# Kernel tuning notes

Hardware: AMD Instinct MI355X
Metric: run time of the kernel (lower is better)

Reference implementation:

```python
import jax, jax.numpy as jnp
import numpy as np

D = 256

def setup_inputs() -> dict:
    key = jax.random.key(0)
    ks = iter(jax.random.split(key, 40))
    def nrm(shape, s=0.05):
        return (jax.random.normal(next(ks), shape, dtype=jnp.float32) * s)
    inp = {}
    inp['prot_data'] = jax.random.normal(next(ks), (8, 1000, 768), dtype=jnp.float32)
    inp['drug_data_ver'] = jax.random.normal(next(ks), (8, 56, 43), dtype=jnp.float32)
    inp['drug_data_adj'] = jax.random.uniform(next(ks), (8, 56, 56), dtype=jnp.float32)
    inp['prot_contacts'] = jax.random.uniform(next(ks), (8, 1000, 1000), dtype=jnp.float32)
    inp['prot_inter'] = jax.random.uniform(next(ks), (8, 1000, 56), dtype=jnp.float32)
    inp['prot_inter_exist'] = jax.random.uniform(next(ks), (8,), dtype=jnp.float32)
    inp['label'] = jax.random.normal(next(ks), (8, 1), dtype=jnp.float32)
    inp['fused_matrix'] = jax.random.normal(next(ks), (999, 1000), dtype=jnp.float32)
    # params
    inp['W_prot'] = nrm((768, D)); inp['b_prot'] = jnp.zeros((D,), jnp.float32)
    inp['gcn_W0'] = nrm((43, D));  inp['gcn_b0'] = jnp.zeros((D,), jnp.float32)
    inp['gcn_W1'] = nrm((D, D));   inp['gcn_b1'] = jnp.zeros((D,), jnp.float32)
    inp['gcn_W2'] = nrm((D, D));   inp['gcn_b2'] = jnp.zeros((D,), jnp.float32)
    inp['gcn_Wf'] = nrm((D, D));   inp['gcn_bf'] = jnp.zeros((D,), jnp.float32)
    inp['Wjp'] = nrm((D, D)); inp['bjp'] = jnp.zeros((D,), jnp.float32)
    inp['Wjc'] = nrm((D, D)); inp['bjc'] = jnp.zeros((D,), jnp.float32)
    inp['conv_w'] = nrm((64, 1, 4)); inp['conv_b'] = jnp.zeros((64,), jnp.float32)
    inp['W_r1'] = nrm((64 * 32, 600)); inp['b_r1'] = jnp.zeros((600,), jnp.float32)
    inp['W_r2'] = nrm((600, 300));     inp['b_r2'] = jnp.zeros((300,), jnp.float32)
    inp['W_r3'] = nrm((300, 1));       inp['b_r3'] = jnp.zeros((1,), jnp.float32)
    return inp

LAM_L1 = 1.0; LAM_FUSED = 1.0; LAM_GROUP = 1.0; LAM_BIND = 1.0

def reference(prot_data, drug_data_ver, drug_data_adj, prot_contacts, prot_inter,
              prot_inter_exist, label, fused_matrix,
              W_prot, b_prot, gcn_W0, gcn_b0, gcn_W1, gcn_b1, gcn_W2, gcn_b2,
              gcn_Wf, gcn_bf, Wjp, bjp, Wjc, bjc, conv_w, conv_b,
              W_r1, b_r1, W_r2, b_r2, W_r3, b_r3):
    # protein embedding (active path: single linear)
    prot = prot_data @ W_prot + b_prot                      # (b, 1000, 256)
    # compound GCN
    x = drug_data_ver
    for W, b in ((gcn_W0, gcn_b0), (gcn_W1, gcn_b1), (gcn_W2, gcn_b2)):
        x = jax.nn.relu(jnp.einsum('bij,bjd->bid', drug_data_adj, x @ W + b))
    comp = x @ gcn_Wf + gcn_bf                              # (b, 56, 256)
    # joint attention over prot x comp
    qp = jax.nn.relu(prot) @ Wjp + bjp
    qc = jax.nn.relu(comp) @ Wjc + bjc
    inter = jax.nn.sigmoid(jnp.einsum('bid,bkd->bik', qp, qc))  # (b, 1000, 56)
    inter = inter / jnp.sum(inter, axis=(1, 2), keepdims=True)
    # outer-product bilinear attention + weighted reduction (the 4D intermediate)
    cp4 = jnp.tanh(prot[:, :, None, :] * comp[:, None, :, :])   # (b, 1000, 56, 256)
    cp = jnp.einsum('bikd,bik->bd', cp4, inter)                 # (b, 256)
    h = cp[:, None, :]                                          # (b, 1, 256) NCH
    h = jax.lax.conv_general_dilated(h, conv_w, (2,), [(1, 1)],
                                     dimension_numbers=('NCH', 'OIH', 'NCH'))
    h = h + conv_b[None, :, None]                               # (b, 64, 128)
    h = jax.nn.leaky_relu(h, 0.1)
    h = jax.lax.reduce_window(h, -jnp.inf, jax.lax.max,
                              (1, 1, 4), (1, 1, 4), 'VALID')    # (b, 64, 32)
    h = h.reshape(h.shape[0], 64 * 32)
    h = jax.nn.leaky_relu(h @ W_r1 + b_r1, 0.1)
    h = jax.nn.leaky_relu(h @ W_r2 + b_r2, 0.1)
    affn = h @ W_r3 + b_r3                                      # (b, 1)
    # losses
    reg_l1 = jnp.mean(jnp.sum(jnp.abs(inter), axis=(1, 2)))
    reg_fused = jnp.mean(jnp.sum(jnp.abs(jnp.einsum('bij,ti->bjt', inter, fused_matrix)), axis=(1, 2)))
    group = jnp.sum(jnp.einsum('bij,bki->bjk', inter ** 2, prot_contacts), axis=1)  # (b, 1000)
    group = jnp.where(group == 0, group + 1e10, group)
    reg_group = jnp.mean(jnp.sum(jnp.sqrt(group) * jnp.sqrt(jnp.sum(prot_contacts, axis=2)), axis=1))
    loss0 = LAM_L1 * reg_l1 + LAM_FUSED * reg_fused + LAM_GROUP * reg_group
    lab_inter = prot_inter_exist[:, None, None] * prot_inter
    loss1 = jnp.mean(jnp.sqrt(jnp.sum((inter - lab_inter) ** 2, axis=(1, 2)))) * LAM_BIND
    loss2 = jnp.mean((affn - label) ** 2)
    return loss0 + loss1 + loss2
```

## Files before the change

### kernel.cpp

```cpp
#include <hip/hip_runtime.h>
#include <hip/hip_bf16.h>
#include <math.h>

#define B 8
#define NP 1000
#define NK 56
#define DP 768
#define DV 43
#define DD 256
#define NT 999

typedef __attribute__((ext_vector_type(8))) short bf16x8;
typedef __attribute__((ext_vector_type(4))) float f32x4;

__device__ inline short f2bf(float x) {
    __hip_bfloat16 h = __float2bfloat16(x);
    return __builtin_bit_cast(short, h);
}


template<bool RELU_IN>
__device__ __forceinline__ void gemm_body(
    const float* __restrict__ A, const short* __restrict__ Wb,
    const float* __restrict__ bias, float* __restrict__ C,
    int N, int K, int bm, int bn, int tid) {
    int lane = tid & 63, w = tid >> 6;
    int m0 = bm * 32 + (w >> 1) * 16;
    int n0 = bn * 128 + (w & 1) * 64;
    int lrow = lane & 15, lk = lane >> 4;
    f32x4 acc[4] = {{0.f,0.f,0.f,0.f},{0.f,0.f,0.f,0.f},
                    {0.f,0.f,0.f,0.f},{0.f,0.f,0.f,0.f}};
    const float* arow = A + (size_t)(m0 + lrow) * K + lk * 8;
    f32x4 a0 = *reinterpret_cast<const f32x4*>(arow);
    f32x4 a1 = *reinterpret_cast<const f32x4*>(arow + 4);
    for (int k0 = 0; k0 < K; k0 += 32) {
        f32x4 c0 = a0, c1 = a1;
        if (k0 + 32 < K) {
            a0 = *reinterpret_cast<const f32x4*>(arow + k0 + 32);
            a1 = *reinterpret_cast<const f32x4*>(arow + k0 + 36);
        }
        bf16x8 af;
        #pragma unroll
        for (int e = 0; e < 4; ++e) {
            float v0 = c0[e], v1 = c1[e];
            if (RELU_IN) { v0 = fmaxf(v0, 0.f); v1 = fmaxf(v1, 0.f); }
            af[e] = f2bf(v0); af[4 + e] = f2bf(v1);
        }
        const short* bbase = Wb + ((size_t)((k0 >> 3) + lk) * N + n0 + lrow) * 8;
        #pragma unroll
        for (int nt = 0; nt < 4; ++nt) {
            bf16x8 bf = *reinterpret_cast<const bf16x8*>(bbase + nt * 128);
            acc[nt] = __builtin_amdgcn_mfma_f32_16x16x32_bf16(af, bf, acc[nt], 0, 0, 0);
        }
    }
    #pragma unroll
    for (int nt = 0; nt < 4; ++nt) {
        int col = n0 + nt * 16 + lrow;
        float bv = bias[col];
        #pragma unroll
        for (int r = 0; r < 4; ++r) {
            int row = m0 + lk * 4 + r;
            C[(size_t)row * N + col] = acc[nt][r] + bv;
        }
    }
}

__device__ __forceinline__ void gcn_layer_body(
    const float* __restrict__ x, const float* __restrict__ adj,
    const float* __restrict__ W, const float* __restrict__ bias,
    float* __restrict__ y, int KIN, int bi, int tid,
    float* arow, float* u) {
    int b = bi / NK, i = bi % NK;
    if (tid < NK) arow[tid] = adj[((size_t)b * NK + i) * NK + tid];
    __syncthreads();
    if (tid < KIN) {
        float a0 = 0.f, a1 = 0.f;
        for (int j = 0; j < NK; j += 2) {
            a0 = fmaf(arow[j],     x[((size_t)b * NK + j)     * KIN + tid], a0);
            a1 = fmaf(arow[j + 1], x[((size_t)b * NK + j + 1) * KIN + tid], a1);
        }
        u[tid] = a0 + a1;
    }
    float rs = 0.f;
    for (int j = 0; j < NK; ++j) rs += arow[j];
    __syncthreads();
    float a0 = 0.f, a1 = 0.f, a2 = 0.f, a3 = 0.f;
    int kk = 0;
    for (; kk + 4 <= KIN; kk += 4) {
        a0 = fmaf(u[kk],     W[(size_t)kk * DD + tid],       a0);
        a1 = fmaf(u[kk + 1], W[(size_t)(kk + 1) * DD + tid], a1);
        a2 = fmaf(u[kk + 2], W[(size_t)(kk + 2) * DD + tid], a2);
        a3 = fmaf(u[kk + 3], W[(size_t)(kk + 3) * DD + tid], a3);
    }
    for (; kk < KIN; ++kk) a0 = fmaf(u[kk], W[(size_t)kk * DD + tid], a0);
    float v = a0 + a1 + a2 + a3 + rs * bias[tid];
    y[((size_t)b * NK + i) * DD + tid] = fmaxf(v, 0.f);
}

__device__ __forceinline__ void gcn_tail_body(
    const float* __restrict__ y1, const float* __restrict__ adj,
    const float* __restrict__ W2, const float* __restrict__ b2,
    const float* __restrict__ Wf, const float* __restrict__ bf,
    const float* __restrict__ Wjc, const float* __restrict__ bjc,
    float* __restrict__ comp, float* __restrict__ qcout,
    int bi, int tid, float* arow, float* u) {
    int b = bi / NK, i = bi % NK;
    if (tid < NK) arow[tid] = adj[((size_t)b * NK + i) * NK + tid];
    __syncthreads();
    {
        float a0 = 0.f, a1 = 0.f;
        for (int j = 0; j < NK; j += 2) {
            a0 = fmaf(arow[j],     y1[((size_t)b * NK + j)     * DD + tid], a0);
            a1 = fmaf(arow[j + 1], y1[((size_t)b * NK + j + 1) * DD + tid], a1);
        }
        u[tid] = a0 + a1;
    }
    float rs = 0.f;
    for (int j = 0; j < NK; ++j) rs += arow[j];
    __syncthreads();
    float a0 = 0.f, a1 = 0.f, a2 = 0.f, a3 = 0.f;
    #pragma unroll 4
    for (int kk = 0; kk < DD; kk += 4) {
        a0 = fmaf(u[kk],     W2[(size_t)kk * DD + tid],       a0);
        a1 = fmaf(u[kk + 1], W2[(size_t)(kk + 1) * DD + tid], a1);
        a2 = fmaf(u[kk + 2], W2[(size_t)(kk + 2) * DD + tid], a2);
        a3 = fmaf(u[kk + 3], W2[(size_t)(kk + 3) * DD + tid], a3);
    }
    float y2 = fmaxf(a0 + a1 + a2 + a3 + rs * b2[tid], 0.f);
    __syncthreads();
    u[tid] = y2;
    __syncthreads();
    a0 = a1 = a2 = a3 = 0.f;
    #pragma unroll 4
    for (int kk = 0; kk < DD; kk += 4) {
        a0 = fmaf(u[kk],     Wf[(size_t)kk * DD + tid],       a0);
        a1 = fmaf(u[kk + 1], Wf[(size_t)(kk + 1) * DD + tid], a1);
        a2 = fmaf(u[kk + 2], Wf[(size_t)(kk + 2) * DD + tid], a2);
        a3 = fmaf(u[kk + 3], Wf[(size_t)(kk + 3) * DD + tid], a3);
    }
    float cv = a0 + a1 + a2 + a3 + bf[tid];
    comp[((size_t)b * NK + i) * DD + tid] = cv;
    __syncthreads();
    u[tid] = fmaxf(cv, 0.f);
    __syncthreads();
    a0 = a1 = a2 = a3 = 0.f;
    #pragma unroll 4
    for (int kk = 0; kk < DD; kk += 4) {
        a0 = fmaf(u[kk],     Wjc[(size_t)kk * DD + tid],       a0);
        a1 = fmaf(u[kk + 1], Wjc[(size_t)(kk + 1) * DD + tid], a1);
        a2 = fmaf(u[kk + 2], Wjc[(size_t)(kk + 2) * DD + tid], a2);
        a3 = fmaf(u[kk + 3], Wjc[(size_t)(kk + 3) * DD + tid], a3);
    }
    qcout[((size_t)b * NK + i) * DD + tid] = a0 + a1 + a2 + a3 + bjc[tid];
}

__global__ __launch_bounds__(256) void k1_kernel(
    const float* __restrict__ W_prot, short* __restrict__ Wb1,
    const float* __restrict__ Wjp, short* __restrict__ Wb2,
    const float* __restrict__ fusedM, short* __restrict__ fMb,
    float* __restrict__ zero_region,
    const float* __restrict__ drug_ver, const float* __restrict__ adj,
    const float* __restrict__ W0, const float* __restrict__ b0,
    float* __restrict__ y0) {
    __shared__ float smem[2112];
    int blk = blockIdx.x, tid = threadIdx.x;
    if (blk < 96) {
        int idx = blk * 256 + tid;
        int koct = idx / DD, n = idx % DD;
        bf16x8 v;
        #pragma unroll
        for (int e = 0; e < 8; ++e)
            v[e] = f2bf(W_prot[(size_t)(koct * 8 + e) * DD + n]);
        *reinterpret_cast<bf16x8*>(Wb1 + (size_t)idx * 8) = v;
    } else if (blk < 128) {
        int idx = (blk - 96) * 256 + tid;
        int koct = idx / DD, n = idx % DD;
        bf16x8 v;
        #pragma unroll
        for (int e = 0; e < 8; ++e)
            v[e] = f2bf(Wjp[(size_t)(koct * 8 + e) * DD + n]);
        *reinterpret_cast<bf16x8*>(Wb2 + (size_t)idx * 8) = v;
    } else if (blk < 640) {
        int blk2 = blk - 128;
        int t0 = (blk2 >> 3) * 16;
        int i0 = (blk2 & 7) * 128;
        for (int l = tid; l < 16 * 128; l += 256) {
            int tt = l >> 7, ii = l & 127;
            int t = t0 + tt, i = i0 + ii;
            smem[tt * 132 + ii] = (t < NT && i < NP) ? fusedM[(size_t)t * NP + i] : 0.f;
        }
        __syncthreads();
        int octl = tid >> 4, tl = tid & 15;
        bf16x8 v;
        #pragma unroll
        for (int e = 0; e < 8; ++e)
            v[e] = f2bf(smem[tl * 132 + octl * 8 + e]);
        size_t oct = i0 / 8 + octl;
        *reinterpret_cast<bf16x8*>(fMb + (oct * 1024 + t0 + tl) * 8) = v;
    } else if (blk < 677) {
        int idx = (blk - 640) * 256 + tid;
        if (idx < 48 + B * 600 + B * 300 + B * DD) zero_region[idx] = 0.f;
    } else {
        gcn_layer_body(drug_ver, adj, W0, b0, y0, DV, blk - 677, tid,
                       smem, smem + 64);
    }
}

__global__ __launch_bounds__(256) void k2_kernel(
    const float* __restrict__ prot_data, const short* __restrict__ Wb1,
    const float* __restrict__ b_prot, float* __restrict__ prot,
    const float* __restrict__ y0, const float* __restrict__ adj,
    const float* __restrict__ W1, const float* __restrict__ b1,
    float* __restrict__ y1) {
    __shared__ float smem[320];
    int blk = blockIdx.x, tid = threadIdx.x;
    if (blk < 500)
        gemm_body<false>(prot_data, Wb1, b_prot, prot, DD, DP, blk >> 1, blk & 1, tid);
    else
        gcn_layer_body(y0, adj, W1, b1, y1, DD, blk - 500, tid, smem, smem + 64);
}

__global__ __launch_bounds__(256) void k3_kernel(
    const float* __restrict__ prot, const short* __restrict__ Wb2,
    const float* __restrict__ bjp, float* __restrict__ qp,
    const float* __restrict__ y1, const float* __restrict__ adj,
    const float* __restrict__ W2, const float* __restrict__ b2,
    const float* __restrict__ Wf, const float* __restrict__ bf,
    const float* __restrict__ Wjc, const float* __restrict__ bjc,
    float* __restrict__ comp, float* __restrict__ qc) {
    __shared__ float smem[320];
    int blk = blockIdx.x, tid = threadIdx.x;
    if (blk < 500)
        gemm_body<true>(prot, Wb2, bjp, qp, DD, DD, blk >> 1, blk & 1, tid);
    else
        gcn_tail_body(y1, adj, W2, b2, Wf, bf, Wjc, bjc, comp, qc,
                      blk - 500, tid, smem, smem + 64);
}

__global__ __launch_bounds__(256) void inter_all_kernel(
    const float* __restrict__ qp, const float* __restrict__ qc,
    const float* __restrict__ prot_inter, const float* __restrict__ exist,
    float* __restrict__ inter, float* __restrict__ s_bi,
    short* __restrict__ iTb, float* __restrict__ accums) {
    int b = blockIdx.x / 125, chunk = blockIdx.x % 125;
    __shared__ float qcT[DD * 57];
    __shared__ float qpS[8][DD];
    __shared__ float vS[8][57];
    __shared__ float wred[4][4];
    int tid = threadIdx.x;
    for (int l = tid; l < NK * DD; l += 256) {
        int k = l / DD, d = l % DD;
        qcT[d * 57 + k] = qc[((size_t)b * NK + k) * DD + d];
    }
    for (int l = tid; l < 8 * DD; l += 256) {
        int r = l >> 8, d = l & 255;
        qpS[r][d] = qp[((size_t)b * NP + chunk * 8 + r) * DD + d];
    }
    __syncthreads();
    int w = tid >> 6, lane = tid & 63;
    float ex = exist[b];
    int r0 = w * 2, r1 = w * 2 + 1;
    float acc0 = 0.f, acc1 = 0.f;
    if (lane < NK) {
        #pragma unroll 8
        for (int d = 0; d < DD; ++d) {
            float c = qcT[d * 57 + lane];
            acc0 = fmaf(qpS[r0][d], c, acc0);
            acc1 = fmaf(qpS[r1][d], c, acc1);
        }
    }
    float aV = 0.f, aA = 0.f, aC = 0.f, aD = 0.f;
    #pragma unroll
    for (int ii = 0; ii < 2; ++ii) {
        int i = chunk * 8 + w * 2 + ii;
        float v = 0.f, lab = 0.f;
        if (lane < NK) {
            float acc = (ii == 0) ? acc0 : acc1;
            v = 1.f / (1.f + __expf(-acc));
            lab = ex * prot_inter[((size_t)b * NP + i) * NK + lane];
            inter[((size_t)b * NP + i) * NK + lane] = v;
            vS[w * 2 + ii][lane] = v;
        }
        float v2 = v * v;
        float r = v2;
        #pragma unroll
        for (int off = 32; off; off >>= 1) r += __shfl_down(r, off);
        if (lane == 0) s_bi[(size_t)b * NP + i] = r;
        aV += v; aA += v2; aC += v * lab; aD += lab * lab;
    }
    #pragma unroll
    for (int off = 32; off; off >>= 1) {
        aV += __shfl_down(aV, off);
        aA += __shfl_down(aA, off);
        aC += __shfl_down(aC, off);
        aD += __shfl_down(aD, off);
    }
    if (lane == 0) {
        wred[w][0] = aV; wred[w][1] = aA; wred[w][2] = aC; wred[w][3] = aD;
    }
    __syncthreads();
    if (tid < 4) {
        float s = wred[0][tid] + wred[1][tid] + wred[2][tid] + wred[3][tid];
        atomicAdd(&accums[tid * 8 + b], s);
    }
    if (tid < NK) {
        bf16x8 pk;
        #pragma unroll
        for (int e = 0; e < 8; ++e) pk[e] = f2bf(vS[e][tid]);
        *reinterpret_cast<bf16x8*>(iTb + ((size_t)chunk * 448 + b * NK + tid) * 8) = pk;
        if (chunk == 124) {
            bf16x8 z = {0,0,0,0,0,0,0,0};
            #pragma unroll
            for (int oct = 125; oct < 128; ++oct)
                *reinterpret_cast<bf16x8*>(iTb + ((size_t)oct * 448 + b * NK + tid) * 8) = z;
        }
    }
}

__global__ __launch_bounds__(256) void k5_kernel(
    const float* __restrict__ prot, const float* __restrict__ comp,
    const float* __restrict__ inter, float* __restrict__ cp,
    const short* __restrict__ iTb, const short* __restrict__ fMb,
    float* __restrict__ fusedAbs,
    const float* __restrict__ contacts, const float* __restrict__ s_bi,
    const float* __restrict__ accums, float* __restrict__ groupv) {
    __shared__ float irow[8][NK];
    __shared__ float sb[8];
    int blk = blockIdx.x, tid = threadIdx.x;
    if (blk < 1000) {
        int b = blk / 125, chunk = blk % 125;
        int d = tid;
        float creg[NK];
        #pragma unroll
        for (int k = 0; k < NK; ++k)
            creg[k] = comp[((size_t)b * NK + k) * DD + d];
        for (int l = tid; l < 8 * NK; l += 256) {
            int ii = l / NK, k = l % NK;
            irow[ii][k] = inter[((size_t)b * NP + chunk * 8 + ii) * NK + k];
        }
        const float C2LOG2E = 2.8853900817779268f;
        float p2l[8];
        #pragma unroll
        for (int ii = 0; ii < 8; ++ii)
            p2l[ii] = C2LOG2E * prot[((size_t)b * NP + chunk * 8 + ii) * DD + d];
        __syncthreads();
        float acc0 = 0.f, acc1 = 0.f;
        #pragma unroll 1
        for (int ii = 0; ii < 8; ++ii) {
            float p = p2l[ii];
            #pragma unroll
            for (int k = 0; k < NK; k += 2) {
                float e0 = __builtin_amdgcn_exp2f(p * creg[k]);
                float e1 = __builtin_amdgcn_exp2f(p * creg[k + 1]);
                float r0 = __builtin_amdgcn_rcpf(e0 + 1.f);
                float r1 = __builtin_amdgcn_rcpf(e1 + 1.f);
                acc0 = fmaf(fmaf(-2.f, r0, 1.f), irow[ii][k],     acc0);
                acc1 = fmaf(fmaf(-2.f, r1, 1.f), irow[ii][k + 1], acc1);
            }
        }
        atomicAdd(&cp[(size_t)b * DD + d], acc0 + acc1);
    } else if (blk < 1112) {
        int fblk = blk - 1000;
        int mb = fblk % 14, nb = fblk / 14;
        int lane = tid & 63, w = tid >> 6;
        if (tid < 8) sb[tid] = 0.f;
        __syncthreads();
        int m0 = mb * 32 + (w >> 1) * 16;
        int n0 = nb * 128 + (w & 1) * 64;
        int lrow = lane & 15, lk = lane >> 4;
        f32x4 acc[4] = {{0.f,0.f,0.f,0.f},{0.f,0.f,0.f,0.f},
                        {0.f,0.f,0.f,0.f},{0.f,0.f,0.f,0.f}};
        for (int koct0 = 0; koct0 < 128; koct0 += 4) {
            int koct = koct0 + lk;
            bf16x8 af = *reinterpret_cast<const bf16x8*>(
                iTb + ((size_t)koct * 448 + m0 + lrow) * 8);
            const short* bb = fMb + ((size_t)koct * 1024 + n0 + lrow) * 8;
            #pragma unroll
            for (int nt = 0; nt < 4; ++nt) {
                bf16x8 bf = *reinterpret_cast<const bf16x8*>(bb + nt * 128);
                acc[nt] = __builtin_amdgcn_mfma_f32_16x16x32_bf16(af, bf, acc[nt], 0, 0, 0);
            }
        }
        #pragma unroll
        for (int r = 0; r < 4; ++r) {
            float part = fabsf(acc[0][r]) + fabsf(acc[1][r]) +
                         fabsf(acc[2][r]) + fabsf(acc[3][r]);
            #pragma unroll
            for (int off = 1; off < 16; off <<= 1)
                part += __shfl_xor(part, off);
            if (lrow == 0) {
                int row = m0 + lk * 4 + r;
                atomicAdd(&sb[row / NK], part);
            }
        }
        __syncthreads();
        if (tid < 8 && sb[tid] != 0.f) atomicAdd(&fusedAbs[tid], sb[tid]);
    } else {
        int w = tid >> 6, lane = tid & 63;
        int gk = (blk - 1112) * 4 + w;
        int b = gk / NP;
        const f32x4* row4 = reinterpret_cast<const f32x4*>(
            contacts + (size_t)gk * NP);
        const f32x4* sv4 = reinterpret_cast<const f32x4*>(s_bi + (size_t)b * NP);
        f32x4 z = {0.f, 0.f, 0.f, 0.f};
        f32x4 c0 = row4[lane];
        f32x4 c1 = row4[lane + 64];
        f32x4 c2 = row4[lane + 128];
        f32x4 c3 = z, s3 = z;
        f32x4 s0 = sv4[lane];
        f32x4 s1 = sv4[lane + 64];
        f32x4 s2 = sv4[lane + 128];
        if (lane + 192 < 250) { c3 = row4[lane + 192]; s3 = sv4[lane + 192]; }
        float g0 = 0.f, g1 = 0.f, g2 = 0.f, g3 = 0.f;
        #pragma unroll
        for (int e = 0; e < 4; ++e) {
            g0 = fmaf(c0[e], s0[e], g0);
            g1 = fmaf(c1[e], s1[e], g1);
            g2 = fmaf(c2[e], s2[e], g2);
            g3 = fmaf(c3[e], s3[e], g3);
        }
        float r0 = (c0[0] + c0[1]) + (c0[2] + c0[3]);
        float r1 = (c1[0] + c1[1]) + (c1[2] + c1[3]);
        float r2 = (c2[0] + c2[1]) + (c2[2] + c2[3]);
        float r3 = (c3[0] + c3[1]) + (c3[2] + c3[3]);
        float g = (g0 + g1) + (g2 + g3);
        float rs = (r0 + r1) + (r2 + r3);
        #pragma unroll
        for (int off = 32; off; off >>= 1) {
            g += __shfl_down(g, off);
            rs += __shfl_down(rs, off);
        }
        if (lane == 0) {
            float val;
            if (g == 0.f) val = sqrtf(1e10f) * sqrtf(rs);
            else          val = sqrtf(g) / accums[b] * sqrtf(rs);
            groupv[gk] = val;
        }
    }
}

__global__ __launch_bounds__(256) void fc1_conv_kernel(
    const float* __restrict__ cp, const float* __restrict__ accums,
    const float* __restrict__ conv_w, const float* __restrict__ conv_b,
    const float* __restrict__ W, float* __restrict__ raw) {
    const int K = 2048, N = 600, kchunk = 128;
    int t = threadIdx.x;
    int ol = t & 63;
    int o = blockIdx.x * 64 + ol;
    int w = t >> 6;
    int kbeg = blockIdx.y * kchunk;
    __shared__ float xS[B][258];
    __shared__ float sin_[B][128];
    for (int l = t; l < B * DD; l += 256) {
        int b = l >> 8, d = l & 255;
        xS[b][d + 1] = cp[(size_t)b * DD + d] / accums[b];
    }
    if (t < B) { xS[t][0] = 0.f; xS[t][257] = 0.f; }
    __syncthreads();
    for (int l = t; l < B * kchunk; l += 256) {
        int b = l >> 7, kl = l & 127;
        int kg = kbeg + kl;
        int oo = kg >> 5, p = kg & 31;
        float w0 = conv_w[oo * 4 + 0], w1 = conv_w[oo * 4 + 1];
        float w2 = conv_w[oo * 4 + 2], w3 = conv_w[oo * 4 + 3];
        float cb = conv_b[oo];
        float m = -INFINITY;
        #pragma unroll
        for (int q = 0; q < 4; ++q) {
            int base = (p * 4 + q) * 2;
            float acc = cb;
            acc = fmaf(xS[b][base + 0], w0, acc);
            acc = fmaf(xS[b][base + 1], w1, acc);
            acc = fmaf(xS[b][base + 2], w2, acc);
            acc = fmaf(xS[b][base + 3], w3, acc);
            acc = (acc > 0.f) ? acc : 0.1f * acc;
            m = fmaxf(m, acc);
        }
        sin_[b][kl] = m;
    }
    __syncthreads();
    float acc[B];
    #pragma unroll
    for (int b = 0; b < B; ++b) acc[b] = 0.f;
    for (int k = kbeg + w; k < kbeg + kchunk; k += 4) {
        float wv = W[(size_t)k * N + o];
        int kl = k - kbeg;
        #pragma unroll
        for (int b = 0; b < B; ++b)
            acc[b] = fmaf(sin_[b][kl], wv, acc[b]);
    }
    __shared__ float red[4][64][B];
    #pragma unroll
    for (int b = 0; b < B; ++b) red[w][ol][b] = acc[b];
    __syncthreads();
    for (int p = t; p < 64 * B; p += 256) {
        int oo = p / B, b = p % B;
        int o2 = blockIdx.x * 64 + oo;
        float s = red[0][oo][b] + red[1][oo][b] + red[2][oo][b] + red[3][oo][b];
        atomicAdd(&raw[(size_t)b * N + o2], s);
    }
}

__global__ __launch_bounds__(256) void fc2_kernel(
    const float* __restrict__ raw1, const float* __restrict__ b_r1,
    const float* __restrict__ W, float* __restrict__ raw2) {
    const int K = 600, N = 300, kchunk = 75;
    int t = threadIdx.x;
    int ol = t & 63;
    int o = blockIdx.x * 64 + ol;
    int w = t >> 6;
    int kbeg = blockIdx.y * kchunk;
    __shared__ float sin_[B][128];
    for (int l = t; l < B * kchunk; l += 256) {
        int b = l / kchunk, k = l % kchunk;
        float v = raw1[(size_t)b * K + kbeg + k] + b_r1[kbeg + k];
        v = (v > 0.f) ? v : 0.1f * v;
        sin_[b][k] = v;
    }
    __syncthreads();
    float acc[B];
    #pragma unroll
    for (int b = 0; b < B; ++b) acc[b] = 0.f;
    if (o < N) {
        for (int k = kbeg + w; k < kbeg + kchunk; k += 4) {
            float wv = W[(size_t)k * N + o];
            int kl = k - kbeg;
            #pragma unroll
            for (int b = 0; b < B; ++b)
                acc[b] = fmaf(sin_[b][kl], wv, acc[b]);
        }
    }
    __shared__ float red[4][64][B];
    #pragma unroll
    for (int b = 0; b < B; ++b) red[w][ol][b] = acc[b];
    __syncthreads();
    for (int p = t; p < 64 * B; p += 256) {
        int oo = p / B, b = p % B;
        int o2 = blockIdx.x * 64 + oo;
        if (o2 < N) {
            float s = red[0][oo][b] + red[1][oo][b] + red[2][oo][b] + red[3][oo][b];
            atomicAdd(&raw2[(size_t)b * N + o2], s);
        }
    }
}

__global__ __launch_bounds__(256) void final_kernel(
    const float* __restrict__ accums, const float* __restrict__ groupv,
    const float* __restrict__ raw2, const float* __restrict__ b_r2,
    const float* __restrict__ W3, const float* __restrict__ b3,
    const float* __restrict__ label, float* __restrict__ out) {
    int tid = threadIdx.x;
    __shared__ float affnS[8];
    {
        int b = tid >> 5, k0 = tid & 31;
        float acc = 0.f;
        for (int k = k0; k < 300; k += 32) {
            float v = raw2[(size_t)b * 300 + k] + b_r2[k];
            v = (v > 0.f) ? v : 0.1f * v;
            acc = fmaf(v, W3[k], acc);
        }
        #pragma unroll
        for (int off = 16; off; off >>= 1) acc += __shfl_down(acc, off);
        if (k0 == 0) affnS[b] = acc + b3[0];
    }
    float s = 0.f;
    for (int l = tid; l < B * NP; l += 256) s += groupv[l];
    __shared__ float r[256];
    r[tid] = s;
    __syncthreads();
    for (int st = 128; st; st >>= 1) {
        if (tid < st) r[tid] += r[tid + st];
        __syncthreads();
    }
    if (tid == 0) {
        float gtot = r[0];
        float l0 = 0.f, l1 = 0.f, l2 = 0.f;
        for (int b = 0; b < B; ++b) {
            float S = accums[b];
            float A = accums[8 + b], C = accums[16 + b], D = accums[24 + b];
            float fA = accums[32 + b];
            l0 += 1.f + fA / S;
            float bind = A / (S * S) - 2.f * C / S + D;
            l1 += sqrtf(fmaxf(bind, 0.f));
            float dd = affnS[b] - label[b];
            l2 += dd * dd;
        }
        out[0] = (l0 + gtot + l1 + l2) * 0.125f;
    }
}

extern "C" void kernel_launch(void* const* d_in, const int* in_sizes, int n_in,
                              void* d_out, int out_size, void* d_ws, size_t ws_size,
                              hipStream_t stream) {
    const float* prot_data   = (const float*)d_in[0];
    const float* drug_ver    = (const float*)d_in[1];
    const float* drug_adj    = (const float*)d_in[2];
    const float* contacts    = (const float*)d_in[3];
    const float* prot_inter  = (const float*)d_in[4];
    const float* exist       = (const float*)d_in[5];
    const float* label       = (const float*)d_in[6];
    const float* fused       = (const float*)d_in[7];
    const float* W_prot      = (const float*)d_in[8];
    const float* b_prot      = (const float*)d_in[9];
    const float* gcn_W0      = (const float*)d_in[10];
    const float* gcn_b0      = (const float*)d_in[11];
    const float* gcn_W1      = (const float*)d_in[12];
    const float* gcn_b1      = (const float*)d_in[13];
    const float* gcn_W2      = (const float*)d_in[14];
    const float* gcn_b2      = (const float*)d_in[15];
    const float* gcn_Wf      = (const float*)d_in[16];
    const float* gcn_bf      = (const float*)d_in[17];
    const float* Wjp         = (const float*)d_in[18];
    const float* bjp         = (const float*)d_in[19];
    const float* Wjc         = (const float*)d_in[20];
    const float* bjc         = (const float*)d_in[21];
    const float* conv_w      = (const float*)d_in[22];
    const float* conv_b      = (const float*)d_in[23];
    const float* W_r1        = (const float*)d_in[24];
    const float* b_r1        = (const float*)d_in[25];
    const float* W_r2        = (const float*)d_in[26];
    const float* b_r2        = (const float*)d_in[27];
    const float* W_r3        = (const float*)d_in[28];
    const float* b_r3        = (const float*)d_in[29];

    float* ws = (float*)d_ws;
    size_t off = 0;
    auto alloc = [&](size_t n) { float* p = ws + off; off += n; return p; };
    float* prot     = alloc((size_t)B * NP * DD);
    float* qp       = alloc((size_t)B * NP * DD);
    float* tbuf     = alloc((size_t)B * NK * DD);
    float* ybuf     = alloc((size_t)B * NK * DD);
    float* comp     = alloc((size_t)B * NK * DD);
    float* qc       = alloc((size_t)B * NK * DD);
    float* inter    = alloc((size_t)B * NP * NK);
    float* s_bi     = alloc((size_t)B * NP);
    float* groupv   = alloc((size_t)B * NP);
    short* Wb1      = (short*)alloc((DP / 8) * DD * 8 / 2);
    short* Wb2      = (short*)alloc((DD / 8) * DD * 8 / 2);
    short* fMb      = (short*)alloc((size_t)128 * 1024 * 8 / 2);
    float* accums   = alloc(48);
    float* raw1     = alloc((size_t)B * 600);
    float* raw2     = alloc((size_t)B * 300);
    float* cp       = alloc((size_t)B * DD);

    short* iTb = (short*)tbuf;
    (void)ybuf;

    k1_kernel<<<1125, 256, 0, stream>>>(W_prot, Wb1, Wjp, Wb2, fused, fMb,
                                        accums, drug_ver, drug_adj,
                                        gcn_W0, gcn_b0, tbuf);

    k2_kernel<<<948, 256, 0, stream>>>(prot_data, Wb1, b_prot, prot,
                                       tbuf, drug_adj, gcn_W1, gcn_b1, ybuf);

    k3_kernel<<<948, 256, 0, stream>>>(prot, Wb2, bjp, qp,
                                       ybuf, drug_adj, gcn_W2, gcn_b2,
                                       gcn_Wf, gcn_bf, Wjc, bjc, comp, qc);

    inter_all_kernel<<<B * 125, 256, 0, stream>>>(
        qp, qc, prot_inter, exist, inter, s_bi, iTb, accums);

    k5_kernel<<<3112, 256, 0, stream>>>(prot, comp, inter, cp,
                                        iTb, fMb, accums + 32,
                                        contacts, s_bi, accums, groupv);

    fc1_conv_kernel<<<dim3(10, 16), 256, 0, stream>>>(
        cp, accums, conv_w, conv_b, W_r1, raw1);

    fc2_kernel<<<dim3(5, 8), 256, 0, stream>>>(raw1, b_r1, W_r2, raw2);

    final_kernel<<<1, 256, 0, stream>>>(accums, groupv, raw2, b_r2,
                                        W_r3, b_r3, label, (float*)d_out);
}
```

Baseline: 160.7 us.

## Compute interaction logits with bf16 MFMA and pre-packed qc layout

Replaces the scalar FMA interaction kernel, which staged transposed qc in shared memory, with an MFMA kernel. The gcn tail now writes qc directly as bf16 in an MFMA-friendly packed layout, with padding zeroed in k1. The launch grid shrinks from 1000 blocks to 128, and each wave computes a 16x64 tile and writes the iTb transposes directly. This trades fp32 precision for bf16 and lowers parallelism, but removes the shared-memory transpose and the scalar dot-product cost.

Result: faster. 143.4 us (-10.8%).

```diff
diff --git a/kernel.cpp b/kernel.cpp
--- a/kernel.cpp
+++ b/kernel.cpp
@@ -17,7 +17,6 @@
     __hip_bfloat16 h = __float2bfloat16(x);
     return __builtin_bit_cast(short, h);
 }
-
 
 template<bool RELU_IN>
 __device__ __forceinline__ void gemm_body(
@@ -102,7 +101,7 @@
     const float* __restrict__ W2, const float* __restrict__ b2,
     const float* __restrict__ Wf, const float* __restrict__ bf,
     const float* __restrict__ Wjc, const float* __restrict__ bjc,
-    float* __restrict__ comp, float* __restrict__ qcout,
+    float* __restrict__ comp, short* __restrict__ qcb,
     int bi, int tid, float* arow, float* u) {
     int b = bi / NK, i = bi % NK;
     if (tid < NK) arow[tid] = adj[((size_t)b * NK + i) * NK + tid];
@@ -151,14 +150,15 @@
         a2 = fmaf(u[kk + 2], Wjc[(size_t)(kk + 2) * DD + tid], a2);
         a3 = fmaf(u[kk + 3], Wjc[(size_t)(kk + 3) * DD + tid], a3);
     }
-    qcout[((size_t)b * NK + i) * DD + tid] = a0 + a1 + a2 + a3 + bjc[tid];
+    float qv = a0 + a1 + a2 + a3 + bjc[tid];
+    qcb[(((size_t)b * 32 + (tid >> 3)) * 64 + i) * 8 + (tid & 7)] = f2bf(qv);
 }
 
 __global__ __launch_bounds__(256) void k1_kernel(
     const float* __restrict__ W_prot, short* __restrict__ Wb1,
     const float* __restrict__ Wjp, short* __restrict__ Wb2,
     const float* __restrict__ fusedM, short* __restrict__ fMb,
-    float* __restrict__ zero_region,
+    float* __restrict__ zero_region, float* __restrict__ qcb_zero,
     const float* __restrict__ drug_ver, const float* __restrict__ adj,
     const float* __restrict__ W0, const float* __restrict__ b0,
     float* __restrict__ y0) {
@@ -200,8 +200,11 @@
     } else if (blk < 677) {
         int idx = (blk - 640) * 256 + tid;
         if (idx < 48 + B * 600 + B * 300 + B * DD) zero_region[idx] = 0.f;
+    } else if (blk < 933) {
+        int idx = (blk - 677) * 256 + tid;
+        qcb_zero[idx] = 0.f;
     } else {
-        gcn_layer_body(drug_ver, adj, W0, b0, y0, DV, blk - 677, tid,
+        gcn_layer_body(drug_ver, adj, W0, b0, y0, DV, blk - 933, tid,
                        smem, smem + 64);
     }
 }
@@ -227,66 +230,84 @@
     const float* __restrict__ W2, const float* __restrict__ b2,
     const float* __restrict__ Wf, const float* __restrict__ bf,
     const float* __restrict__ Wjc, const float* __restrict__ bjc,
-    float* __restrict__ comp, float* __restrict__ qc) {
+    float* __restrict__ comp, short* __restrict__ qcb) {
     __shared__ float smem[320];
     int blk = blockIdx.x, tid = threadIdx.x;
     if (blk < 500)
         gemm_body<true>(prot, Wb2, bjp, qp, DD, DD, blk >> 1, blk & 1, tid);
     else
-        gcn_tail_body(y1, adj, W2, b2, Wf, bf, Wjc, bjc, comp, qc,
+        gcn_tail_body(y1, adj, W2, b2, Wf, bf, Wjc, bjc, comp, qcb,
                       blk - 500, tid, smem, smem + 64);
 }
 
-__global__ __launch_bounds__(256) void inter_all_kernel(
-    const float* __restrict__ qp, const float* __restrict__ qc,
+__global__ __launch_bounds__(256) void inter_mfma_kernel(
+    const float* __restrict__ qp, const short* __restrict__ qcb,
     const float* __restrict__ prot_inter, const float* __restrict__ exist,
     float* __restrict__ inter, float* __restrict__ s_bi,
     short* __restrict__ iTb, float* __restrict__ accums) {
-    int b = blockIdx.x / 125, chunk = blockIdx.x % 125;
-    __shared__ float qcT[DD * 57];
-    __shared__ float qpS[8][DD];
-    __shared__ float vS[8][57];
     __shared__ float wred[4][4];
+    int blk = blockIdx.x;
+    int b = blk >> 4, mt = blk & 15;
     int tid = threadIdx.x;
-    for (int l = tid; l < NK * DD; l += 256) {
-        int k = l / DD, d = l % DD;
-        qcT[d * 57 + k] = qc[((size_t)b * NK + k) * DD + d];
-    }
-    for (int l = tid; l < 8 * DD; l += 256) {
-        int r = l >> 8, d = l & 255;
-        qpS[r][d] = qp[((size_t)b * NP + chunk * 8 + r) * DD + d];
-    }
-    __syncthreads();
-    int w = tid >> 6, lane = tid & 63;
+    int lane = tid & 63, w = tid >> 6;
+    int m0 = mt * 64 + w * 16;
+    int lrow = lane & 15, lk = lane >> 4;
+    f32x4 acc[4] = {{0.f,0.f,0.f,0.f},{0.f,0.f,0.f,0.f},
+                    {0.f,0.f,0.f,0.f},{0.f,0.f,0.f,0.f}};
+    int rowi = m0 + lrow;
+    int rowc = (rowi < NP) ? rowi : (NP - 1);
+    const float* arow = qp + ((size_t)b * NP + rowc) * DD + lk * 8;
+    f32x4 a0 = *reinterpret_cast<const f32x4*>(arow);
+    f32x4 a1 = *reinterpret_cast<const f32x4*>(arow + 4);
+    for (int k0 = 0; k0 < DD; k0 += 32) {
+        f32x4 c0 = a0, c1 = a1;
+        if (k0 + 32 < DD) {
+            a0 = *reinterpret_cast<const f32x4*>(arow + k0 + 32);
+            a1 = *reinterpret_cast<const f32x4*>(arow + k0 + 36);
+        }
+        bf16x8 af;
+        #pragma unroll
+        for (int e = 0; e < 4; ++e) {
+            af[e] = f2bf(c0[e]); af[4 + e] = f2bf(c1[e]);
+        }
+        const short* bb = qcb + (((size_t)b * 32 + (k0 >> 3) + lk) * 64 + lrow) * 8;
+        #pragma unroll
+        for (int nt = 0; nt < 4; ++nt) {
+            bf16x8 bf = *reinterpret_cast<const bf16x8*>(bb + nt * 128);
+            acc[nt] = __builtin_amdgcn_mfma_f32_16x16x32_bf16(af, bf, acc[nt], 0, 0, 0);
+        }
+    }
     float ex = exist[b];
-    int r0 = w * 2, r1 = w * 2 + 1;
-    float acc0 = 0.f, acc1 = 0.f;
-    if (lane < NK) {
-        #pragma unroll 8
-        for (int d = 0; d < DD; ++d) {
-            float c = qcT[d * 57 + lane];
-            acc0 = fmaf(qpS[r0][d], c, acc0);
-            acc1 = fmaf(qpS[r1][d], c, acc1);
-        }
-    }
     float aV = 0.f, aA = 0.f, aC = 0.f, aD = 0.f;
-    #pragma unroll
-    for (int ii = 0; ii < 2; ++ii) {
-        int i = chunk * 8 + w * 2 + ii;
-        float v = 0.f, lab = 0.f;
-        if (lane < NK) {
-            float acc = (ii == 0) ? acc0 : acc1;
-            v = 1.f / (1.f + __expf(-acc));
-            lab = ex * prot_inter[((size_t)b * NP + i) * NK + lane];
-            inter[((size_t)b * NP + i) * NK + lane] = v;
-            vS[w * 2 + ii][lane] = v;
-        }
-        float v2 = v * v;
-        float r = v2;
-        #pragma unroll
-        for (int off = 32; off; off >>= 1) r += __shfl_down(r, off);
-        if (lane == 0) s_bi[(size_t)b * NP + i] = r;
-        aV += v; aA += v2; aC += v * lab; aD += lab * lab;
+    float rowsq[4] = {0.f, 0.f, 0.f, 0.f};
+    #pragma unroll
+    for (int nt = 0; nt < 4; ++nt) {
+        int j = nt * 16 + lrow;
+        bool jv = (j < NK);
+        #pragma unroll
+        for (int r = 0; r < 4; ++r) {
+            int i = m0 + lk * 4 + r;
+            bool iv = (i < NP);
+            float v = 0.f, lab = 0.f;
+            if (jv) {
+                if (iv) {
+                    v = 1.f / (1.f + __expf(-acc[nt][r]));
+                    lab = ex * prot_inter[((size_t)b * NP + i) * NK + j];
+                    inter[((size_t)b * NP + i) * NK + j] = v;
+                }
+                iTb[(((size_t)(i >> 3) * 448 + b * NK + j) << 3) + (i & 7)] = f2bf(v);
+            }
+            aV += v; aA += v * v; aC += v * lab; aD += lab * lab;
+            rowsq[r] += v * v;
+        }
+    }
+    #pragma unroll
+    for (int r = 0; r < 4; ++r) {
+        float rs = rowsq[r];
+        rs += __shfl_xor(rs, 1); rs += __shfl_xor(rs, 2);
+        rs += __shfl_xor(rs, 4); rs += __shfl_xor(rs, 8);
+        int i = m0 + lk * 4 + r;
+        if (lrow == 0 && i < NP) s_bi[(size_t)b * NP + i] = rs;
     }
     #pragma unroll
     for (int off = 32; off; off >>= 1) {
@@ -302,18 +323,6 @@
     if (tid < 4) {
         float s = wred[0][tid] + wred[1][tid] + wred[2][tid] + wred[3][tid];
         atomicAdd(&accums[tid * 8 + b], s);
-    }
-    if (tid < NK) {
-        bf16x8 pk;
-        #pragma unroll
-        for (int e = 0; e < 8; ++e) pk[e] = f2bf(vS[e][tid]);
-        *reinterpret_cast<bf16x8*>(iTb + ((size_t)chunk * 448 + b * NK + tid) * 8) = pk;
-        if (chunk == 124) {
-            bf16x8 z = {0,0,0,0,0,0,0,0};
-            #pragma unroll
-            for (int oct = 125; oct < 128; ++oct)
-                *reinterpret_cast<bf16x8*>(iTb + ((size_t)oct * 448 + b * NK + tid) * 8) = z;
-        }
     }
 }
 
@@ -443,7 +452,7 @@
     const float* __restrict__ cp, const float* __restrict__ accums,
     const float* __restrict__ conv_w, const float* __restrict__ conv_b,
     const float* __restrict__ W, float* __restrict__ raw) {
-    const int K = 2048, N = 600, kchunk = 128;
+    const int N = 600, kchunk = 128;
     int t = threadIdx.x;
     int ol = t & 63;
     int o = blockIdx.x * 64 + ol;
@@ -631,7 +640,7 @@
     float* tbuf     = alloc((size_t)B * NK * DD);
     float* ybuf     = alloc((size_t)B * NK * DD);
     float* comp     = alloc((size_t)B * NK * DD);
-    float* qc       = alloc((size_t)B * NK * DD);
+    float* qcbF     = alloc((size_t)65536);
     float* inter    = alloc((size_t)B * NP * NK);
     float* s_bi     = alloc((size_t)B * NP);
     float* groupv   = alloc((size_t)B * NP);
@@ -643,11 +652,12 @@
     float* raw2     = alloc((size_t)B * 300);
     float* cp       = alloc((size_t)B * DD);
 
+    short* qcb = (short*)qcbF;
     short* iTb = (short*)tbuf;
     (void)ybuf;
 
-    k1_kernel<<<1125, 256, 0, stream>>>(W_prot, Wb1, Wjp, Wb2, fused, fMb,
-                                        accums, drug_ver, drug_adj,
+    k1_kernel<<<1381, 256, 0, stream>>>(W_prot, Wb1, Wjp, Wb2, fused, fMb,
+                                        accums, qcbF, drug_ver, drug_adj,
                                         gcn_W0, gcn_b0, tbuf);
 
     k2_kernel<<<948, 256, 0, stream>>>(prot_data, Wb1, b_prot, prot,
@@ -655,10 +665,10 @@
 
     k3_kernel<<<948, 256, 0, stream>>>(prot, Wb2, bjp, qp,
                                        ybuf, drug_adj, gcn_W2, gcn_b2,
-                                       gcn_Wf, gcn_bf, Wjc, bjc, comp, qc);
-
-    inter_all_kernel<<<B * 125, 256, 0, stream>>>(
-        qp, qc, prot_inter, exist, inter, s_bi, iTb, accums);
+                                       gcn_Wf, gcn_bf, Wjc, bjc, comp, qcb);
+
+    inter_mfma_kernel<<<128, 256, 0, stream>>>(
+        qp, qcb, prot_inter, exist, inter, s_bi, iTb, accums);
 
     k5_kernel<<<3112, 256, 0, stream>>>(prot, comp, inter, cp,
                                         iTb, fMb, accums + 32,
```
